# Performance work log

Measured on AMD Instinct MI355X. Metric: run time of the kernel, lower is better.

The kernel has to match this reference:

```python
import jax, jax.numpy as jnp
import numpy as np

B, C, Q = 16, 1024, 128
XD, YD = 64, 32
D, H, HID, L = 512, 8, 2048, 6
HD = D // H
NEG = -1e9


def setup_inputs() -> dict:
    key = jax.random.key(0)
    ks = jax.random.split(key, 12)
    rn = lambda k, shape, s: jax.random.normal(k, shape, jnp.float32) * s
    return {
        "x_c": rn(ks[0], (B, C, XD), 1.0),
        "y_c": rn(ks[1], (B, C, YD), 1.0),
        "x_q": rn(ks[2], (B, Q, XD), 1.0),
        "W_val": rn(ks[3], (XD + YD, D), (XD + YD) ** -0.5),
        "b_val": jnp.zeros((D,), jnp.float32),
        "q_emb": rn(ks[4], (D,), D ** -0.5),
        "in_proj_w": rn(ks[5], (L, 3 * D, D), D ** -0.5),
        "in_proj_b": jnp.zeros((L, 3 * D), jnp.float32),
        "out_w": rn(ks[6], (L, D, D), D ** -0.5),
        "out_b": jnp.zeros((L, D), jnp.float32),
        "ln1_g": jnp.ones((L, D), jnp.float32),
        "ln1_b": jnp.zeros((L, D), jnp.float32),
        "lin1_w": rn(ks[7], (L, HID, D), D ** -0.5),
        "lin1_b": jnp.zeros((L, HID), jnp.float32),
        "lin2_w": rn(ks[8], (L, D, HID), HID ** -0.5),
        "lin2_b": jnp.zeros((L, D), jnp.float32),
        "ln2_g": jnp.ones((L, D), jnp.float32),
        "ln2_b": jnp.zeros((L, D), jnp.float32),
        "W_head": rn(ks[9], (D, YD), D ** -0.5),
        "b_head": jnp.zeros((YD,), jnp.float32),
    }


def _layernorm(x, g, b):
    mu = x.mean(-1, keepdims=True)
    var = ((x - mu) ** 2).mean(-1, keepdims=True)
    return (x - mu) * jax.lax.rsqrt(var + 1e-5) * g + b


def _forward(x_c, y_c, x_q, W_val, b_val, q_emb, in_proj_w, in_proj_b, out_w,
             out_b, ln1_g, ln1_b, lin1_w, lin1_b, lin2_w, lin2_b, ln2_g, ln2_b,
             W_head, b_head):
    bsz, c_len, _ = x_c.shape
    q_len = x_q.shape[1]
    S = c_len + q_len
    # concat y onto x; queries get zero y placeholder
    xy_c = jnp.concatenate([x_c, y_c], axis=-1)
    xy_q = jnp.concatenate([x_q, jnp.zeros((bsz, q_len, y_c.shape[-1]), x_q.dtype)], axis=-1)
    xy = jnp.concatenate([xy_c, xy_q], axis=1) @ W_val + b_val          # [B,S,D]
    xy = xy.at[:, -q_len:].add(q_emb)
    # src_mask: no one may attend to query positions (last q_len keys)
    bias = jnp.where(jnp.arange(S) >= c_len, jnp.float32(NEG), jnp.float32(0.0))  # [S] key axis

    def layer(x, p):
        ipw, ipb, ow, ob, g1, b1, w1, bb1, w2, bb2, g2, b2 = p
        qkv = x @ ipw.T + ipb                                           # [B,S,3D]
        q, k, v = jnp.split(qkv, 3, axis=-1)
        heads = lambda t: t.reshape(bsz, S, H, HD).transpose(0, 2, 1, 3)  # [B,H,S,HD]
        q, k, v = heads(q), heads(k), heads(v)
        scores = jnp.einsum('bhqd,bhkd->bhqk', q, k) / np.float32(np.sqrt(HD)) + bias
        attn = jax.nn.softmax(scores, axis=-1)
        ctx = jnp.einsum('bhqk,bhkd->bhqd', attn, v)
        ctx = ctx.transpose(0, 2, 1, 3).reshape(bsz, S, D)
        x = _layernorm(x + ctx @ ow.T + ob, g1, b1)                     # post-norm
        ff = jax.nn.relu(x @ w1.T + bb1) @ w2.T + bb2
        x = _layernorm(x + ff, g2, b2)
        return x, None

    params = (in_proj_w, in_proj_b, out_w, out_b, ln1_g, ln1_b,
              lin1_w, lin1_b, lin2_w, lin2_b, ln2_g, ln2_b)
    x, _ = jax.lax.scan(layer, xy, params)
    return x[:, -q_len:] @ W_head + b_head                              # [B,Q,YD]


def reference(x_c, y_c, x_q, W_val, b_val, q_emb, in_proj_w, in_proj_b, out_w,
              out_b, ln1_g, ln1_b, lin1_w, lin1_b, lin2_w, lin2_b, ln2_g, ln2_b,
              W_head, b_head):
    return _forward(x_c, y_c, x_q, W_val, b_val, q_emb, in_proj_w, in_proj_b,
                    out_w, out_b, ln1_g, ln1_b, lin1_w, lin1_b, lin2_w, lin2_b,
                    ln2_g, ln2_b, W_head, b_head)
```

## Files before the change

kernel.cpp:

```cpp
#include <hip/hip_runtime.h>

#define B_   16
#define C_   1024
#define Q_   128
#define S_   1152
#define D_   512
#define H_   8
#define HID_ 2048
#define L_   6
#define M_   (B_*S_)
#define MQ_  (B_*Q_)
#define QSC_ 0.18033688011f

typedef short bf16x8 __attribute__((ext_vector_type(8)));
typedef float f32x4  __attribute__((ext_vector_type(4)));
#define MFMA16(a,b,c) __builtin_amdgcn_mfma_f32_16x16x32_bf16(a,b,c,0,0,0)

__device__ __forceinline__ unsigned short f2b(float f){
  union { float f; unsigned u; } v; v.f = f;
  return (unsigned short)((v.u + 0x7FFF + ((v.u >> 16) & 1)) >> 16);
}
__device__ __forceinline__ float b2f(unsigned short u){
  return __uint_as_float((unsigned)u << 16);
}
__device__ __forceinline__ void gload16(const void* g, void* l){
  __builtin_amdgcn_global_load_lds((const __attribute__((address_space(1))) void*)g,
                                   (__attribute__((address_space(3))) void*)l, 16, 0, 0);
}
__device__ __forceinline__ float waveSum(float v){
  #pragma unroll
  for (int o = 32; o > 0; o >>= 1) v += __shfl_down(v, o, 64);
  return v;
}

__global__ __launch_bounds__(256) void f2b_kernel(
    const float* __restrict__ in, unsigned short* __restrict__ out, int n4)
{
  int i = blockIdx.x*256 + threadIdx.x;
  for (; i < n4; i += gridDim.x*256) {
    float4 v = ((const float4*)in)[i];
    ushort4 o = { f2b(v.x), f2b(v.y), f2b(v.z), f2b(v.w) };
    ((ushort4*)out)[i] = o;
  }
}

__global__ __launch_bounds__(256) void f2bq_kernel(
    const float* __restrict__ in, unsigned short* __restrict__ out, int n4)
{
  int i = blockIdx.x*256 + threadIdx.x;
  for (; i < n4; i += gridDim.x*256) {
    const int row = (i >> 7) % 1536;
    const float s = (row < 512) ? QSC_ : 1.f;
    float4 v = ((const float4*)in)[i];
    ushort4 o = { f2b(v.x*s), f2b(v.y*s), f2b(v.z*s), f2b(v.w*s) };
    ((ushort4*)out)[i] = o;
  }
}

__global__ __launch_bounds__(256) void sbias_kernel(
    const float* __restrict__ in, float* __restrict__ out)
{
  int idx = blockIdx.x*256 + threadIdx.x;
  if (idx < L_*1536) {
    int j = idx % 1536;
    out[idx] = in[idx] * (j < 512 ? QSC_ : 1.f);
  }
}

__global__ __launch_bounds__(256) void packxy_kernel(
    const float* __restrict__ x_c, const float* __restrict__ y_c,
    const float* __restrict__ x_q, unsigned short* __restrict__ XY)
{
  int idx = blockIdx.x*256 + threadIdx.x;
  const int n = M_*128;
  for (; idx < n; idx += gridDim.x*256) {
    int row = idx >> 7, col = idx & 127;
    int bb = row / S_, s = row % S_;
    float v;
    if (col < 64) {
      v = (s < C_) ? x_c[((size_t)bb*C_ + s)*64 + col]
                   : x_q[((size_t)bb*Q_ + (s - C_))*64 + col];
    } else if (col < 96) {
      v = (s < C_) ? y_c[((size_t)bb*C_ + s)*32 + (col - 64)] : 0.f;
    } else if (col == 96) {
      v = 1.f;
    } else if (col == 97) {
      v = (s >= C_) ? 1.f : 0.f;
    } else v = 0.f;
    XY[idx] = f2b(v);
  }
}

__global__ __launch_bounds__(256) void wemb_kernel(
    const float* __restrict__ W_val, const float* __restrict__ b_val,
    const float* __restrict__ q_emb, unsigned short* __restrict__ Wemb)
{
  int idx = blockIdx.x*256 + threadIdx.x;
  int nn = idx >> 7, k = idx & 127;
  float v;
  if (k < 96)       v = W_val[k*D_ + nn];
  else if (k == 96) v = b_val[nn];
  else if (k == 97) v = q_emb[nn];
  else              v = 0.f;
  Wemb[idx] = f2b(v);
}

__global__ __launch_bounds__(256) void gatherq_kernel(
    const unsigned short* __restrict__ X, unsigned short* __restrict__ Xq)
{
  int row = blockIdx.x;
  int bb = row >> 7, qi = row & 127;
  const unsigned short* src = X + ((size_t)bb*S_ + C_ + qi)*D_;
  unsigned short* dst = Xq + (size_t)row*D_;
  int tid = threadIdx.x;
  dst[tid] = src[tid];
  dst[tid + 256] = src[tid + 256];
}

#define SWZ(row) (((row) >> 1) & 3)

template<int RELU, int BOUT>
__global__ __launch_bounds__(256) void bgemm_kernel(
    const unsigned short* __restrict__ A, const unsigned short* __restrict__ W,
    const float* __restrict__ bias,
    float* __restrict__ Cf, unsigned short* __restrict__ Cb, int Nn, int Kk)
{
  __shared__ short As[2][4096];
  __shared__ short Bs[2][4096];
  int lin = blockIdx.y * gridDim.x + blockIdx.x;
  const int nwg = gridDim.x * gridDim.y;
  const int cpx = nwg >> 3;
  lin = (lin & 7) * cpx + (lin >> 3);
  const int bm = (lin / gridDim.x) * 128, bn = (lin % gridDim.x) * 128;

  const int tid = threadIdx.x;
  const int w = tid >> 6, lane = tid & 63, l15 = lane & 15, l4 = lane >> 4;
  const int wm = w >> 1, wn = w & 1;
  f32x4 acc[4][4] = {};
  const size_t strA = (size_t)Kk * 2;
  const char* Abase = (const char*)A + (size_t)bm * strA;
  const char* Wbase = (const char*)W + (size_t)bn * strA;
  const int srow = tid >> 2;
  const int schunk = (tid & 3) ^ SWZ(srow);
  const size_t soff = (size_t)srow * strA + (size_t)(schunk * 16);
  const int ldsOff = w * 1024;

#define STAGEK(K0, BUF) do { \
    const char* a0_ = Abase + soff + (size_t)(K0)*2; \
    const char* b0_ = Wbase + soff + (size_t)(K0)*2; \
    char* la_ = (char*)As + (BUF)*8192 + ldsOff; \
    char* lb_ = (char*)Bs + (BUF)*8192 + ldsOff; \
    gload16(a0_,            la_); \
    gload16(a0_ + 64*strA,  la_ + 4096); \
    gload16(b0_,            lb_); \
    gload16(b0_ + 64*strA,  lb_ + 4096); \
  } while(0)

  STAGEK(0, 0);
  const int nk = Kk >> 5;
  for (int t = 0; t < nk; t++) {
    __syncthreads();
    if (t + 1 < nk) STAGEK((t+1)*32, (t+1)&1);
    const short* AsC = (const short*)As + (t&1)*4096;
    const short* BsC = (const short*)Bs + (t&1)*4096;
    bf16x8 af[4], bfr[4];
    #pragma unroll
    for (int mf = 0; mf < 4; mf++) {
      const int ar = wm*64 + mf*16 + l15;
      af[mf] = *(const bf16x8*)(AsC + ar*32 + (l4 ^ SWZ(ar))*8);
    }
    #pragma unroll
    for (int nf = 0; nf < 4; nf++) {
      const int br = wn*64 + nf*16 + l15;
      bfr[nf] = *(const bf16x8*)(BsC + br*32 + (l4 ^ SWZ(br))*8);
    }
    #pragma unroll
    for (int mf = 0; mf < 4; mf++)
      #pragma unroll
      for (int nf = 0; nf < 4; nf++)
        acc[mf][nf] = MFMA16(af[mf], bfr[nf], acc[mf][nf]);
  }
#undef STAGEK

  #pragma unroll
  for (int mf = 0; mf < 4; mf++) {
    #pragma unroll
    for (int nf = 0; nf < 4; nf++) {
      const int ccol = bn + wn*64 + nf*16 + l15;
      const float bv = bias[ccol];
      #pragma unroll
      for (int r = 0; r < 4; r++) {
        const int rrow = bm + wm*64 + mf*16 + l4*4 + r;
        float o = acc[mf][nf][r] + bv;
        if (RELU) o = fmaxf(o, 0.f);
        if (BOUT == 1) Cb[(size_t)rrow*Nn + ccol] = f2b(o);
        else           Cf[(size_t)rrow*Nn + ccol] = o;
      }
    }
  }
}

__global__ __launch_bounds__(256) void bgemm64_kernel(
    const unsigned short* __restrict__ A, const unsigned short* __restrict__ W,
    const float* __restrict__ bias, const unsigned short* __restrict__ Rsd,
    float* __restrict__ Cf, int Nn, int Kk)
{
  __shared__ short As[3][4096];
  __shared__ short Bs[3][2048];
  int lin = blockIdx.y * gridDim.x + blockIdx.x;
  const int nwg = gridDim.x * gridDim.y;
  const int cpx = nwg >> 3;
  lin = (lin & 7) * cpx + (lin >> 3);
  const int bm = (lin / gridDim.x) * 128, bn = (lin % gridDim.x) * 64;

  const int tid = threadIdx.x;
  const int w = tid >> 6, lane = tid & 63, l15 = lane & 15, l4 = lane >> 4;
  f32x4 acc[2][4] = {};
  const size_t strA = (size_t)Kk * 2;
  const char* Abase = (const char*)A + (size_t)bm * strA;
  const char* Wbase = (const char*)W + (size_t)bn * strA;
  const int srow = tid >> 2;
  const int schunk = (tid & 3) ^ SWZ(srow);
  const size_t soff = (size_t)srow * strA + (size_t)(schunk * 16);
  const int ldsOff = w * 1024;

#define STAGEK64(K0, BUF) do { \
    const char* a0_ = Abase + soff + (size_t)(K0)*2; \
    const char* b0_ = Wbase + soff + (size_t)(K0)*2; \
    char* la_ = (char*)As + (BUF)*8192 + ldsOff; \
    char* lb_ = (char*)Bs + (BUF)*4096 + ldsOff; \
    gload16(a0_,            la_); \
    gload16(a0_ + 64*strA,  la_ + 4096); \
    gload16(b0_,            lb_); \
  } while(0)

  const int nk = Kk >> 5;
  STAGEK64(0, 0);
  STAGEK64(32, 1);
  int rb = 0;
  for (int t = 0; t < nk; t++) {
    if (t + 1 < nk) asm volatile("s_waitcnt vmcnt(3)" ::: "memory");
    else            asm volatile("s_waitcnt vmcnt(0)" ::: "memory");
    __builtin_amdgcn_s_barrier();
    __builtin_amdgcn_sched_barrier(0);
    if (t + 2 < nk) {
      int wbuf = rb + 2; if (wbuf >= 3) wbuf -= 3;
      STAGEK64((t+2)*32, wbuf);
    }
    const short* AsC = (const short*)As + rb*4096;
    const short* BsC = (const short*)Bs + rb*2048;
    bf16x8 af[2], bfr[4];
    #pragma unroll
    for (int mf = 0; mf < 2; mf++) {
      const int ar = w*32 + mf*16 + l15;
      af[mf] = *(const bf16x8*)(AsC + ar*32 + (l4 ^ SWZ(ar))*8);
    }
    #pragma unroll
    for (int nf = 0; nf < 4; nf++) {
      const int br = nf*16 + l15;
      bfr[nf] = *(const bf16x8*)(BsC + br*32 + (l4 ^ SWZ(br))*8);
    }
    #pragma unroll
    for (int mf = 0; mf < 2; mf++)
      #pragma unroll
      for (int nf = 0; nf < 4; nf++)
        acc[mf][nf] = MFMA16(af[mf], bfr[nf], acc[mf][nf]);
    rb++; if (rb >= 3) rb = 0;
  }
#undef STAGEK64

  #pragma unroll
  for (int mf = 0; mf < 2; mf++) {
    #pragma unroll
    for (int nf = 0; nf < 4; nf++) {
      const int ccol = bn + nf*16 + l15;
      const float bv = bias[ccol];
      #pragma unroll
      for (int r = 0; r < 4; r++) {
        const int rrow = bm + w*32 + mf*16 + l4*4 + r;
        float o = acc[mf][nf][r] + bv + b2f(Rsd[(size_t)rrow*Nn + ccol]);
        Cf[(size_t)rrow*Nn + ccol] = o;
      }
    }
  }
}

__global__ __launch_bounds__(256) void mattn_kernel(
    const unsigned short* __restrict__ QKV, unsigned short* __restrict__ Ctx,
    int nqt, int qoff, int orows)
{
  __shared__ short Ks[64*72];
  __shared__ short Vt[64*72];
  __shared__ short Ps[4*16*72];
  int bid = blockIdx.x;
  const int nwg = gridDim.x;
  bid = (bid & 7) * (nwg >> 3) + (bid >> 3);
  const int qt = bid % nqt;
  const int h  = (bid / nqt) % H_;
  const int bb = bid / (nqt*H_);
  const int tid = threadIdx.x;
  const int w = tid >> 6, lane = tid & 63, l15 = lane & 15, l4 = lane >> 4;

  const size_t rowQ = (size_t)bb*S_ + qoff + (size_t)qt*64 + w*16 + l15;
  const unsigned short* qp = QKV + rowQ*1536 + h*64;
  const bf16x8 qf0 = *(const bf16x8*)(qp + l4*8);
  const bf16x8 qf1 = *(const bf16x8*)(qp + 32 + l4*8);

  const unsigned short* Kg = QKV + (size_t)bb*S_*1536 + 512 + h*64;
  const unsigned short* Vg = Kg + 512;

  f32x4 ctx[4] = {};
  f32x4 lacc = {};
  float m_r[4];
  #pragma unroll
  for (int r = 0; r < 4; r++) m_r[r] = -3.0e38f;

  const bf16x8 onesv = {(short)0x3F80,(short)0x3F80,(short)0x3F80,(short)0x3F80,
                        (short)0x3F80,(short)0x3F80,(short)0x3F80,(short)0x3F80};

  char* PsW = (char*)Ps + w*2304;

  const int skey = tid >> 3, shc = tid & 7;
  const int vp   = tid >> 3, vhc = tid & 7;

  const unsigned short* gK = Kg + (size_t)skey*1536 + shc*8;
  const unsigned short* gV = Vg + (size_t)(2*vp)*1536 + vhc*8;
  bf16x8 k0v = *(const bf16x8*)gK;
  bf16x8 k1v = *(const bf16x8*)(gK + 32*1536);
  bf16x8 c0  = *(const bf16x8*)gV;
  bf16x8 c1  = *(const bf16x8*)(gV + 1536);

  for (int kt = 0; kt < 16; kt++) {
    __syncthreads();
    *(bf16x8*)((char*)Ks + skey*144      + shc*16) = k0v;
    *(bf16x8*)((char*)Ks + (skey+32)*144 + shc*16) = k1v;
    #pragma unroll
    for (int j = 0; j < 8; j++) {
      const int hd = vhc*8 + j;
      unsigned int val = (unsigned int)(unsigned short)c0[j]
                       | ((unsigned int)(unsigned short)c1[j] << 16);
      *(unsigned int*)((char*)Vt + hd*144 + ((4*vp) ^ (vhc<<4))) = val;
    }
    __syncthreads();
    if (kt < 15) {
      const unsigned short* nK = gK + (size_t)(kt+1)*98304;
      const unsigned short* nV = gV + (size_t)(kt+1)*98304;
      k0v = *(const bf16x8*)nK;
      k1v = *(const bf16x8*)(nK + 32*1536);
      c0  = *(const bf16x8*)nV;
      c1  = *(const bf16x8*)(nV + 1536);
    }

    f32x4 sac[4] = {};
    __builtin_amdgcn_s_setprio(1);
    #pragma unroll
    for (int nf = 0; nf < 4; nf++) {
      const char* kb = (char*)Ks + (nf*16 + l15)*144 + l4*16;
      bf16x8 b0 = *(const bf16x8*)kb;
      bf16x8 b1 = *(const bf16x8*)(kb + 64);
      sac[nf] = MFMA16(qf0, b0, sac[nf]);
      sac[nf] = MFMA16(qf1, b1, sac[nf]);
    }
    __builtin_amdgcn_s_setprio(0);

    float lmax[4];
    #pragma unroll
    for (int r = 0; r < 4; r++)
      lmax[r] = fmaxf(fmaxf(sac[0][r], sac[1][r]), fmaxf(sac[2][r], sac[3][r]));
    int ok = 1;
    #pragma unroll
    for (int r = 0; r < 4; r++) ok &= (lmax[r] <= m_r[r] + 11.5409f) ? 1 : 0;
    if (!__all(ok)) {
      #pragma unroll
      for (int r = 0; r < 4; r++) {
        float t = lmax[r];
        t = fmaxf(t, __shfl_xor(t, 1, 64));
        t = fmaxf(t, __shfl_xor(t, 2, 64));
        t = fmaxf(t, __shfl_xor(t, 4, 64));
        t = fmaxf(t, __shfl_xor(t, 8, 64));
        const float mn = fmaxf(m_r[r], t);
        const float scl = __builtin_amdgcn_exp2f(m_r[r] - mn);
        m_r[r] = mn;
        lacc[r] *= scl;
        ctx[0][r] *= scl; ctx[1][r] *= scl;
        ctx[2][r] *= scl; ctx[3][r] *= scl;
      }
    }
    #pragma unroll
    for (int r = 0; r < 4; r++) {
      unsigned short* pw = (unsigned short*)(PsW + (l4*4 + r)*144);
      const float m0 = m_r[r];
      pw[ 0 + l15] = (unsigned short)(__float_as_uint(__builtin_amdgcn_exp2f(sac[0][r] - m0)) >> 16);
      pw[16 + l15] = (unsigned short)(__float_as_uint(__builtin_amdgcn_exp2f(sac[1][r] - m0)) >> 16);
      pw[32 + l15] = (unsigned short)(__float_as_uint(__builtin_amdgcn_exp2f(sac[2][r] - m0)) >> 16);
      pw[48 + l15] = (unsigned short)(__float_as_uint(__builtin_amdgcn_exp2f(sac[3][r] - m0)) >> 16);
    }

    const char* pb = PsW + l15*144 + l4*16;
    const bf16x8 pf0 = *(const bf16x8*)pb;
    const bf16x8 pf1 = *(const bf16x8*)(pb + 64);
    __builtin_amdgcn_s_setprio(1);
    lacc = MFMA16(pf0, onesv, lacc);
    lacc = MFMA16(pf1, onesv, lacc);
    #pragma unroll
    for (int hf = 0; hf < 4; hf++) {
      const int hd = hf*16 + l15;
      const int hc = (hd >> 3) & 7;
      const char* vb = (char*)Vt + hd*144;
      bf16x8 v0 = *(const bf16x8*)(vb + ((l4*16)     ^ (hc<<4)));
      bf16x8 v1 = *(const bf16x8*)(vb + (((l4+4)*16) ^ (hc<<4)));
      ctx[hf] = MFMA16(pf0, v0, ctx[hf]);
      ctx[hf] = MFMA16(pf1, v1, ctx[hf]);
    }
    __builtin_amdgcn_s_setprio(0);
  }

  #pragma unroll
  for (int r = 0; r < 4; r++) {
    const float invl = 1.0f / lacc[r];
    const size_t row = (size_t)bb*orows + (size_t)qt*64 + w*16 + l4*4 + r;
    unsigned short* op = Ctx + row*512 + h*64;
    op[ 0 + l15] = f2b(ctx[0][r]*invl);
    op[16 + l15] = f2b(ctx[1][r]*invl);
    op[32 + l15] = f2b(ctx[2][r]*invl);
    op[48 + l15] = f2b(ctx[3][r]*invl);
  }
}

__global__ __launch_bounds__(256) void ln_kernel(
    const float* __restrict__ Yin, const float* __restrict__ g, const float* __restrict__ b,
    unsigned short* __restrict__ Xb)
{
  int row = blockIdx.x, tid = threadIdx.x;
  const float* yr = Yin + (size_t)row*D_;
  float v0 = yr[tid], v1 = yr[tid + 256];
  __shared__ float red[4];
  float s = waveSum(v0 + v1);
  if ((tid & 63) == 0) red[tid >> 6] = s;
  __syncthreads();
  float mu = (red[0] + red[1] + red[2] + red[3]) * (1.f/512.f);
  __syncthreads();
  float d0 = v0 - mu, d1 = v1 - mu;
  float ss = waveSum(d0*d0 + d1*d1);
  if ((tid & 63) == 0) red[tid >> 6] = ss;
  __syncthreads();
  float inv = rsqrtf((red[0] + red[1] + red[2] + red[3]) * (1.f/512.f) + 1e-5f);
  Xb[(size_t)row*D_ + tid]       = f2b(d0 * inv * g[tid]       + b[tid]);
  Xb[(size_t)row*D_ + tid + 256] = f2b(d1 * inv * g[tid + 256] + b[tid + 256]);
}

__global__ __launch_bounds__(64) void head_kernel(
    const unsigned short* __restrict__ Xq, const float* __restrict__ W_head,
    const float* __restrict__ b_head, float* __restrict__ out)
{
  int row = blockIdx.x;
  const unsigned short* xr = Xq + (size_t)row*D_;
  __shared__ float xs[512];
  int tid = threadIdx.x;
  for (int i = tid; i < 512; i += 64) xs[i] = b2f(xr[i]);
  __syncthreads();
  if (tid < 32) {
    float acc = b_head[tid];
    #pragma unroll 8
    for (int k = 0; k < 512; k++) acc += xs[k] * W_head[k*32 + tid];
    out[(size_t)row*32 + tid] = acc;
  }
}

extern "C" void kernel_launch(void* const* d_in, const int* in_sizes, int n_in,
                              void* d_out, int out_size, void* d_ws, size_t ws_size,
                              hipStream_t stream)
{
  const float* x_c      = (const float*)d_in[0];
  const float* y_c      = (const float*)d_in[1];
  const float* x_q      = (const float*)d_in[2];
  const float* W_val    = (const float*)d_in[3];
  const float* b_val    = (const float*)d_in[4];
  const float* q_emb    = (const float*)d_in[5];
  const float* in_proj_w= (const float*)d_in[6];
  const float* in_proj_b= (const float*)d_in[7];
  const float* out_w    = (const float*)d_in[8];
  const float* out_b    = (const float*)d_in[9];
  const float* ln1_g    = (const float*)d_in[10];
  const float* ln1_b    = (const float*)d_in[11];
  const float* lin1_w   = (const float*)d_in[12];
  const float* lin1_b   = (const float*)d_in[13];
  const float* lin2_w   = (const float*)d_in[14];
  const float* lin2_b   = (const float*)d_in[15];
  const float* ln2_g    = (const float*)d_in[16];
  const float* ln2_b    = (const float*)d_in[17];
  const float* W_head   = (const float*)d_in[18];
  const float* b_head   = (const float*)d_in[19];
  float* out = (float*)d_out;

  char* p = (char*)d_ws;
  float* Yf = (float*)p;                     p += (size_t)M_*D_*4;
  unsigned short* hid  = (unsigned short*)p; p += (size_t)M_*HID_*2;
  unsigned short* Xb2  = (unsigned short*)p; p += (size_t)M_*D_*2;
  unsigned short* qkv  = (unsigned short*)p; p += (size_t)M_*3*D_*2;
  unsigned short* Xb1  = qkv;
  unsigned short* ctxb = (unsigned short*)p; p += (size_t)M_*D_*2;
  unsigned short* ipwB = (unsigned short*)p; p += (size_t)L_*3*D_*D_*2;
  unsigned short* owB  = (unsigned short*)p; p += (size_t)L_*D_*D_*2;
  unsigned short* w1B  = (unsigned short*)p; p += (size_t)L_*HID_*D_*2;
  unsigned short* w2B  = (unsigned short*)p; p += (size_t)L_*D_*HID_*2;
  unsigned short* XYb  = (unsigned short*)p; p += (size_t)M_*128*2;
  unsigned short* Wemb = (unsigned short*)p; p += (size_t)D_*128*2;
  float* zbias         = (float*)p;          p += 2048*4;
  float* qkvbias       = (float*)p;          p += L_*1536*4;

  unsigned short* ctxq  = ctxb;
  float*          Yfq   = Yf;
  unsigned short* hidq  = hid;
  unsigned short* Xqb2  = XYb;
  unsigned short* Xqb1  = XYb + (size_t)MQ_*D_;

  (void)hipMemsetAsync(zbias, 0, 2048*4, stream);

  f2bq_kernel<<<512, 256, 0, stream>>>(in_proj_w, ipwB, L_*3*D_*D_/4);
  sbias_kernel<<<36, 256, 0, stream>>>(in_proj_b, qkvbias);
  f2b_kernel<<<512, 256, 0, stream>>>(out_w,     owB,  L_*D_*D_/4);
  f2b_kernel<<<512, 256, 0, stream>>>(lin1_w,    w1B,  L_*HID_*D_/4);
  f2b_kernel<<<512, 256, 0, stream>>>(lin2_w,    w2B,  L_*D_*HID_/4);
  wemb_kernel<<<256, 256, 0, stream>>>(W_val, b_val, q_emb, Wemb);
  packxy_kernel<<<1024, 256, 0, stream>>>(x_c, y_c, x_q, XYb);

  bgemm_kernel<0,1><<<dim3(4, 144), 256, 0, stream>>>(
      XYb, Wemb, zbias, nullptr, Xb2, D_, 128);

  for (int l = 0; l < L_ - 1; l++) {
    bgemm_kernel<0,1><<<dim3(12, 144), 256, 0, stream>>>(
        Xb2, ipwB + (size_t)l*3*D_*D_, qkvbias + (size_t)l*3*D_,
        nullptr, qkv, 3*D_, D_);
    mattn_kernel<<<B_*H_*18, 256, 0, stream>>>(qkv, ctxb, 18, 0, S_);
    bgemm64_kernel<<<dim3(8, 144), 256, 0, stream>>>(
        ctxb, owB + (size_t)l*D_*D_, out_b + (size_t)l*D_, Xb2, Yf, D_, D_);
    ln_kernel<<<M_, 256, 0, stream>>>(Yf, ln1_g + (size_t)l*D_, ln1_b + (size_t)l*D_, Xb1);
    bgemm_kernel<1,1><<<dim3(16, 144), 256, 0, stream>>>(
        Xb1, w1B + (size_t)l*HID_*D_, lin1_b + (size_t)l*HID_,
        nullptr, hid, HID_, D_);
    bgemm64_kernel<<<dim3(8, 144), 256, 0, stream>>>(
        hid, w2B + (size_t)l*D_*HID_, lin2_b + (size_t)l*D_, Xb1, Yf, D_, HID_);
    ln_kernel<<<M_, 256, 0, stream>>>(Yf, ln2_g + (size_t)l*D_, ln2_b + (size_t)l*D_, Xb2);
  }

  {
    const int l = L_ - 1;
    bgemm_kernel<0,1><<<dim3(12, 144), 256, 0, stream>>>(
        Xb2, ipwB + (size_t)l*3*D_*D_, qkvbias + (size_t)l*3*D_,
        nullptr, qkv, 3*D_, D_);
    mattn_kernel<<<B_*H_*2, 256, 0, stream>>>(qkv, ctxq, 2, C_, Q_);
    gatherq_kernel<<<MQ_, 256, 0, stream>>>(Xb2, Xqb2);
    bgemm64_kernel<<<dim3(8, 16), 256, 0, stream>>>(
        ctxq, owB + (size_t)l*D_*D_, out_b + (size_t)l*D_, Xqb2, Yfq, D_, D_);
    ln_kernel<<<MQ_, 256, 0, stream>>>(Yfq, ln1_g + (size_t)l*D_, ln1_b + (size_t)l*D_, Xqb1);
    bgemm_kernel<1,1><<<dim3(16, 16), 256, 0, stream>>>(
        Xqb1, w1B + (size_t)l*HID_*D_, lin1_b + (size_t)l*HID_,
        nullptr, hidq, HID_, D_);
    bgemm64_kernel<<<dim3(8, 16), 256, 0, stream>>>(
        hidq, w2B + (size_t)l*D_*HID_, lin2_b + (size_t)l*D_, Xqb1, Yfq, D_, HID_);
    ln_kernel<<<MQ_, 256, 0, stream>>>(Yfq, ln2_g + (size_t)l*D_, ln2_b + (size_t)l*D_, Xqb2);
  }

  head_kernel<<<MQ_, 64, 0, stream>>>(Xqb2, W_head, b_head, out);
}
```

Baseline: 1.753 ms.

## Split-K the FFN down-projection GEMM and fuse partial-sum reduction into layernorm

Replaces the 128x64-tile FFN second GEMM (K=2048) with a 128x128-tile split-K kernel that divides K into two halves, writing the first half (with bias and residual) and the second half into separate fp32 buffers. A new layernorm kernel adds the two partials before normalizing. The aim is larger tiles with more operand reuse while keeping enough workgroups to fill the GPU. The cost is an extra fp32 M×D buffer write and read, stored in the unused tail of the qkv workspace.

```diff
diff --git a/kernel.cpp b/kernel.cpp
--- a/kernel.cpp
+++ b/kernel.cpp
@@ -200,6 +200,92 @@
   }
 }
 
+__global__ __launch_bounds__(256) void bgemm_sk_kernel(
+    const unsigned short* __restrict__ A, const unsigned short* __restrict__ W,
+    const float* __restrict__ bias, const unsigned short* __restrict__ Rsd,
+    float* __restrict__ C0, float* __restrict__ C1, int Nn, int Kfull)
+{
+  __shared__ short As[2][4096];
+  __shared__ short Bs[2][4096];
+  int lin = blockIdx.y * gridDim.x + blockIdx.x;
+  const int nwg = gridDim.x * gridDim.y;
+  const int cpx = nwg >> 3;
+  lin = (lin & 7) * cpx + (lin >> 3);
+  int rowblk = lin / gridDim.x;
+  const int bn = (lin % gridDim.x) * 128;
+  const int z = (rowblk >= 144) ? 1 : 0;
+  if (z) rowblk -= 144;
+  const int bm = rowblk * 128;
+  const int KS = Kfull >> 1;
+
+  const int tid = threadIdx.x;
+  const int w = tid >> 6, lane = tid & 63, l15 = lane & 15, l4 = lane >> 4;
+  const int wm = w >> 1, wn = w & 1;
+  f32x4 acc[4][4] = {};
+  const size_t strA = (size_t)Kfull * 2;
+  const char* Abase = (const char*)A + (size_t)bm * strA + (size_t)z*KS*2;
+  const char* Wbase = (const char*)W + (size_t)bn * strA + (size_t)z*KS*2;
+  const int srow = tid >> 2;
+  const int schunk = (tid & 3) ^ SWZ(srow);
+  const size_t soff = (size_t)srow * strA + (size_t)(schunk * 16);
+  const int ldsOff = w * 1024;
+
+#define STAGEK(K0, BUF) do { \
+    const char* a0_ = Abase + soff + (size_t)(K0)*2; \
+    const char* b0_ = Wbase + soff + (size_t)(K0)*2; \
+    char* la_ = (char*)As + (BUF)*8192 + ldsOff; \
+    char* lb_ = (char*)Bs + (BUF)*8192 + ldsOff; \
+    gload16(a0_,            la_); \
+    gload16(a0_ + 64*strA,  la_ + 4096); \
+    gload16(b0_,            lb_); \
+    gload16(b0_ + 64*strA,  lb_ + 4096); \
+  } while(0)
+
+  STAGEK(0, 0);
+  const int nk = KS >> 5;
+  for (int t = 0; t < nk; t++) {
+    __syncthreads();
+    if (t + 1 < nk) STAGEK((t+1)*32, (t+1)&1);
+    const short* AsC = (const short*)As + (t&1)*4096;
+    const short* BsC = (const short*)Bs + (t&1)*4096;
+    bf16x8 af[4], bfr[4];
+    #pragma unroll
+    for (int mf = 0; mf < 4; mf++) {
+      const int ar = wm*64 + mf*16 + l15;
+      af[mf] = *(const bf16x8*)(AsC + ar*32 + (l4 ^ SWZ(ar))*8);
+    }
+    #pragma unroll
+    for (int nf = 0; nf < 4; nf++) {
+      const int br = wn*64 + nf*16 + l15;
+      bfr[nf] = *(const bf16x8*)(BsC + br*32 + (l4 ^ SWZ(br))*8);
+    }
+    #pragma unroll
+    for (int mf = 0; mf < 4; mf++)
+      #pragma unroll
+      for (int nf = 0; nf < 4; nf++)
+        acc[mf][nf] = MFMA16(af[mf], bfr[nf], acc[mf][nf]);
+  }
+#undef STAGEK
+
+  #pragma unroll
+  for (int mf = 0; mf < 4; mf++) {
+    #pragma unroll
+    for (int nf = 0; nf < 4; nf++) {
+      const int ccol = bn + wn*64 + nf*16 + l15;
+      #pragma unroll
+      for (int r = 0; r < 4; r++) {
+        const int rrow = bm + wm*64 + mf*16 + l4*4 + r;
+        if (z == 0) {
+          C0[(size_t)rrow*Nn + ccol] = acc[mf][nf][r] + bias[ccol]
+                                     + b2f(Rsd[(size_t)rrow*Nn + ccol]);
+        } else {
+          C1[(size_t)rrow*Nn + ccol] = acc[mf][nf][r];
+        }
+      }
+    }
+  }
+}
+
 __global__ __launch_bounds__(256) void bgemm64_kernel(
     const unsigned short* __restrict__ A, const unsigned short* __restrict__ W,
     const float* __restrict__ bias, const unsigned short* __restrict__ Rsd,
@@ -434,6 +520,31 @@
   int row = blockIdx.x, tid = threadIdx.x;
   const float* yr = Yin + (size_t)row*D_;
   float v0 = yr[tid], v1 = yr[tid + 256];
+  __shared__ float red[4];
+  float s = waveSum(v0 + v1);
+  if ((tid & 63) == 0) red[tid >> 6] = s;
+  __syncthreads();
+  float mu = (red[0] + red[1] + red[2] + red[3]) * (1.f/512.f);
+  __syncthreads();
+  float d0 = v0 - mu, d1 = v1 - mu;
+  float ss = waveSum(d0*d0 + d1*d1);
+  if ((tid & 63) == 0) red[tid >> 6] = ss;
+  __syncthreads();
+  float inv = rsqrtf((red[0] + red[1] + red[2] + red[3]) * (1.f/512.f) + 1e-5f);
+  Xb[(size_t)row*D_ + tid]       = f2b(d0 * inv * g[tid]       + b[tid]);
+  Xb[(size_t)row*D_ + tid + 256] = f2b(d1 * inv * g[tid + 256] + b[tid + 256]);
+}
+
+__global__ __launch_bounds__(256) void lnsum_kernel(
+    const float* __restrict__ Y0, const float* __restrict__ Y1,
+    const float* __restrict__ g, const float* __restrict__ b,
+    unsigned short* __restrict__ Xb)
+{
+  int row = blockIdx.x, tid = threadIdx.x;
+  const float* y0 = Y0 + (size_t)row*D_;
+  const float* y1 = Y1 + (size_t)row*D_;
+  float v0 = y0[tid] + y1[tid];
+  float v1 = y0[tid + 256] + y1[tid + 256];
   __shared__ float red[4];
   float s = waveSum(v0 + v1);
   if ((tid & 63) == 0) red[tid >> 6] = s;
@@ -499,6 +610,7 @@
   unsigned short* Xb2  = (unsigned short*)p; p += (size_t)M_*D_*2;
   unsigned short* qkv  = (unsigned short*)p; p += (size_t)M_*3*D_*2;
   unsigned short* Xb1  = qkv;
+  float* Yf1 = (float*)(qkv + (size_t)M_*D_);
   unsigned short* ctxb = (unsigned short*)p; p += (size_t)M_*D_*2;
   unsigned short* ipwB = (unsigned short*)p; p += (size_t)L_*3*D_*D_*2;
   unsigned short* owB  = (unsigned short*)p; p += (size_t)L_*D_*D_*2;
@@ -539,9 +651,9 @@
     bgemm_kernel<1,1><<<dim3(16, 144), 256, 0, stream>>>(
         Xb1, w1B + (size_t)l*HID_*D_, lin1_b + (size_t)l*HID_,
         nullptr, hid, HID_, D_);
-    bgemm64_kernel<<<dim3(8, 144), 256, 0, stream>>>(
-        hid, w2B + (size_t)l*D_*HID_, lin2_b + (size_t)l*D_, Xb1, Yf, D_, HID_);
-    ln_kernel<<<M_, 256, 0, stream>>>(Yf, ln2_g + (size_t)l*D_, ln2_b + (size_t)l*D_, Xb2);
+    bgemm_sk_kernel<<<dim3(4, 288), 256, 0, stream>>>(
+        hid, w2B + (size_t)l*D_*HID_, lin2_b + (size_t)l*D_, Xb1, Yf, Yf1, D_, HID_);
+    lnsum_kernel<<<M_, 256, 0, stream>>>(Yf, Yf1, ln2_g + (size_t)l*D_, ln2_b + (size_t)l*D_, Xb2);
   }
 
   {
```

Measured after the change: 1.809 ms. 3.2% more time.
